# Optimization experiments

Measured on AMD Instinct MI355X. Metric: run time of the kernel, lower is better.

Reference implementation:

```python
import jax, jax.numpy as jnp
import numpy as np

B, N2, N3, D = 16, 1024, 2048, 128


def setup_inputs() -> dict:
    key = jax.random.key(0)
    k1, k2 = jax.random.split(key)
    desc2d = jax.random.normal(k1, (B * N2, D), dtype=jnp.float32)
    desc3d = jax.random.normal(k2, (B * N3, D), dtype=jnp.float32)
    # uniform, sorted batch ids (equal-size segments -> jit-friendly ragged layout)
    idx2d = jnp.repeat(jnp.arange(B, dtype=jnp.int64), N2)
    idx3d = jnp.repeat(jnp.arange(B, dtype=jnp.int64), N3)
    return {"desc2d": desc2d, "idx2d": idx2d, "desc3d": desc3d, "idx3d": idx3d}


def reference(desc2d, idx2d, desc3d, idx3d):
    # number of batches from sorted batch ids (static, computed on host)
    nb = int(np.asarray(idx2d)[-1]) + 1
    n2 = desc2d.shape[0] // nb
    n3 = desc3d.shape[0] // nb
    d2 = desc2d.reshape(nb, n2, -1)  # [B, n2, D]
    d3 = desc3d.reshape(nb, n3, -1)  # [B, n3, D]
    d2 = d2 / jnp.linalg.norm(d2, axis=-1, keepdims=True)
    d3 = d3 / jnp.linalg.norm(d3, axis=-1, keepdims=True)
    sim = jnp.einsum('bid,bjd->bij', d3, d2)  # cosine similarity [B, n3, n2]
    # zero-pad one extra row and column per batch (dustbin), as in the original
    return jnp.pad(sim, ((0, 0), (0, 1), (0, 1)))
```

## Files before the change

kernel.cpp:

```cpp
#include <hip/hip_runtime.h>
#include <hip/hip_bf16.h>

#define NB   16
#define N2   1024
#define N3   2048
#define DD   128
#define OROWS (N3 + 1)
#define OCOLS (N2 + 1)

typedef __attribute__((ext_vector_type(8))) __bf16 bf16x8;
typedef __attribute__((ext_vector_type(4))) float  f32x4;

static __device__ __forceinline__ unsigned pack_bf16x2(float a, float b) {
    unsigned ua = __float_as_uint(a);
    ua = (ua + 0x7FFF + ((ua >> 16) & 1)) >> 16;
    unsigned ub = __float_as_uint(b);
    ub = (ub + 0x7FFF + ((ub >> 16) & 1)) & 0xFFFF0000u;
    return ua | ub;
}

__global__ __launch_bounds__(512, 1)
void fused_kernel(const float* __restrict__ d2,
                  const float* __restrict__ d3,
                  float* __restrict__ out) {
    __shared__ __align__(16) char smem[65536];

    const int hw  = blockIdx.x;
    const int blk = (hw & 7) * 32 + (hw >> 3);
    const int b   = blk >> 4;
    const int ti  = blk & 15;

    const int t = threadIdx.x;

    const float* gA = d3 + ((size_t)(b * N3 + ti * 128)) * DD;
    const float* gB = d2 + ((size_t)b * N2) * DD;

    const int arow  = t >> 2;
    const int apart = t & 3;
    float4 av[8];
    #pragma unroll
    for (int i = 0; i < 8; ++i)
        av[i] = *reinterpret_cast<const float4*>(gA + (size_t)arow * DD + apart * 32 + i * 4);

    const int brow  = t >> 3;
    const int bpart = t & 7;
    float4 bv[4];
    #pragma unroll
    for (int i = 0; i < 4; ++i)
        bv[i] = *reinterpret_cast<const float4*>(gB + (size_t)brow * DD + bpart * 16 + i * 4);

    {
        float ss = 0.f;
        #pragma unroll
        for (int i = 0; i < 8; ++i)
            ss += av[i].x * av[i].x + av[i].y * av[i].y + av[i].z * av[i].z + av[i].w * av[i].w;
        ss += __shfl_xor(ss, 1);
        ss += __shfl_xor(ss, 2);
        const float s = rsqrtf(ss);
        const int aswz = (arow & 7) << 4;
        #pragma unroll
        for (int j = 0; j < 4; ++j) {
            uint4 w;
            w.x = pack_bf16x2(av[2*j].x * s,   av[2*j].y * s);
            w.y = pack_bf16x2(av[2*j].z * s,   av[2*j].w * s);
            w.z = pack_bf16x2(av[2*j+1].x * s, av[2*j+1].y * s);
            w.w = pack_bf16x2(av[2*j+1].z * s, av[2*j+1].w * s);
            int colb = apart * 64 + j * 16;
            *reinterpret_cast<uint4*>(smem + arow * 256 + (colb ^ aswz)) = w;
        }
    }
    {
        float ss = 0.f;
        #pragma unroll
        for (int i = 0; i < 4; ++i)
            ss += bv[i].x * bv[i].x + bv[i].y * bv[i].y + bv[i].z * bv[i].z + bv[i].w * bv[i].w;
        ss += __shfl_xor(ss, 1);
        ss += __shfl_xor(ss, 2);
        ss += __shfl_xor(ss, 4);
        const float s = rsqrtf(ss);
        const int bswz = (brow & 7) << 4;
        #pragma unroll
        for (int j = 0; j < 2; ++j) {
            uint4 w;
            w.x = pack_bf16x2(bv[2*j].x * s,   bv[2*j].y * s);
            w.y = pack_bf16x2(bv[2*j].z * s,   bv[2*j].w * s);
            w.z = pack_bf16x2(bv[2*j+1].x * s, bv[2*j+1].y * s);
            w.w = pack_bf16x2(bv[2*j+1].z * s, bv[2*j+1].w * s);
            int colb = bpart * 32 + j * 16;
            *reinterpret_cast<uint4*>(smem + 32768 + brow * 256 + (colb ^ bswz)) = w;
        }
    }
    asm volatile("s_waitcnt lgkmcnt(0)" ::: "memory");
    __builtin_amdgcn_s_barrier();
    __builtin_amdgcn_sched_barrier(0);

    const int wid = t >> 6;
    const int l   = t & 63;
    const int wm  = (wid >> 2) * 64;
    const int wn  = (wid & 3) * 16;
    const int lr  = l & 15;
    const int kq  = l >> 4;
    const int sw  = (lr & 7) << 4;

    bf16x8 af[4][4];
    #pragma unroll
    for (int ks = 0; ks < 4; ++ks) {
        const int kb = ks * 64 + kq * 16;
        #pragma unroll
        for (int mi = 0; mi < 4; ++mi) {
            int r = wm + mi * 16 + lr;
            af[ks][mi] = *reinterpret_cast<const bf16x8*>(smem + r * 256 + (kb ^ sw));
        }
    }

    float* obase = out + (size_t)b * OROWS * OCOLS + (size_t)(ti * 128) * OCOLS;

    for (int nj = 0; nj < 16; ++nj) {
        if (nj < 15) {
            const float* gc = gB + (size_t)(nj + 1) * 64 * DD;
            #pragma unroll
            for (int i = 0; i < 4; ++i)
                bv[i] = *reinterpret_cast<const float4*>(gc + (size_t)brow * DD + bpart * 16 + i * 4);
        }

        const char* bbuf = smem + 32768 + (nj & 1) * 16384;
        f32x4 acc[4] = {};
        #pragma unroll
        for (int ks = 0; ks < 4; ++ks) {
            const int kb = ks * 64 + kq * 16;
            bf16x8 bfr = *reinterpret_cast<const bf16x8*>(bbuf + (wn + lr) * 256 + (kb ^ sw));
            #pragma unroll
            for (int mi = 0; mi < 4; ++mi)
                acc[mi] = __builtin_amdgcn_mfma_f32_16x16x32_bf16(
                    af[ks][mi], bfr, acc[mi], 0, 0, 0);
        }

        #pragma unroll
        for (int mi = 0; mi < 4; ++mi) {
            #pragma unroll
            for (int i = 0; i < 4; ++i) {
                int r = wm + mi * 16 + kq * 4 + i;
                int c = nj * 64 + wn + lr;
                obase[(size_t)r * OCOLS + c] = acc[mi][i];
            }
        }

        if (nj < 15) {
            float ss = 0.f;
            #pragma unroll
            for (int i = 0; i < 4; ++i)
                ss += bv[i].x * bv[i].x + bv[i].y * bv[i].y + bv[i].z * bv[i].z + bv[i].w * bv[i].w;
            ss += __shfl_xor(ss, 1);
            ss += __shfl_xor(ss, 2);
            ss += __shfl_xor(ss, 4);
            const float s = rsqrtf(ss);
            const int bswz = (brow & 7) << 4;
            char* nb = smem + 32768 + ((nj + 1) & 1) * 16384;
            #pragma unroll
            for (int j = 0; j < 2; ++j) {
                uint4 w;
                w.x = pack_bf16x2(bv[2*j].x * s,   bv[2*j].y * s);
                w.y = pack_bf16x2(bv[2*j].z * s,   bv[2*j].w * s);
                w.z = pack_bf16x2(bv[2*j+1].x * s, bv[2*j+1].y * s);
                w.w = pack_bf16x2(bv[2*j+1].z * s, bv[2*j+1].w * s);
                int colb = bpart * 32 + j * 16;
                *reinterpret_cast<uint4*>(nb + brow * 256 + (colb ^ bswz)) = w;
            }
            asm volatile("s_waitcnt lgkmcnt(0)" ::: "memory");
        }
        asm volatile("" ::: "memory");
        __builtin_amdgcn_s_barrier();
        __builtin_amdgcn_sched_barrier(0);
    }

    if (t < 128)
        obase[(size_t)t * OCOLS + N2] = 0.0f;
    if (ti == 15) {
        float* last = out + (size_t)b * OROWS * OCOLS + (size_t)N3 * OCOLS;
        for (int c = t; c < OCOLS; c += 512) last[c] = 0.0f;
    }
}

extern "C" void kernel_launch(void* const* d_in, const int* in_sizes, int n_in,
                              void* d_out, int out_size, void* d_ws, size_t ws_size,
                              hipStream_t stream) {
    (void)in_sizes; (void)n_in; (void)out_size; (void)d_ws; (void)ws_size;
    const float* desc2d = (const float*)d_in[0];
    const float* desc3d = (const float*)d_in[2];
    float* out = (float*)d_out;

    fused_kernel<<<NB * (N3 / 128), 512, 0, stream>>>(desc2d, desc3d, out);
}
```

Before: 44.03 us.

## Load B fragments directly into registers, removing LDS staging and per-tile barriers

Each lane now loads its own B-operand slice straight from global memory in MFMA fragment layout. It normalizes the slice with a cross-lane shuffle reduction and packs it to bf16 in registers, so the B tile no longer goes through LDS. This removes the per-iteration LDS writes, the lgkmcnt waits and the workgroup barriers, and halves the LDS footprint. In exchange, each of the two waves sharing a wn column slice loads and normalizes the same B rows, doubling B global traffic (mostly L2 hits). The loop is unrolled by two with register double buffering, which raises register pressure.

```diff
diff --git a/kernel.cpp b/kernel.cpp
--- a/kernel.cpp
+++ b/kernel.cpp
@@ -23,17 +23,25 @@
 void fused_kernel(const float* __restrict__ d2,
                   const float* __restrict__ d3,
                   float* __restrict__ out) {
-    __shared__ __align__(16) char smem[65536];
+    __shared__ __align__(16) char smem[32768];
 
     const int hw  = blockIdx.x;
     const int blk = (hw & 7) * 32 + (hw >> 3);
     const int b   = blk >> 4;
     const int ti  = blk & 15;
+    const int t   = threadIdx.x;
 
-    const int t = threadIdx.x;
+    const int wid = t >> 6;
+    const int l   = t & 63;
+    const int wm  = (wid >> 2) * 64;
+    const int wn  = (wid & 3) * 16;
+    const int lr  = l & 15;
+    const int kq  = l >> 4;
+    const int sw  = (lr & 7) << 4;
 
-    const float* gA = d3 + ((size_t)(b * N3 + ti * 128)) * DD;
-    const float* gB = d2 + ((size_t)b * N2) * DD;
+    const float* gA  = d3 + ((size_t)(b * N3 + ti * 128)) * DD;
+    const float* gB  = d2 + ((size_t)b * N2) * DD;
+    const float* gBl = gB + (size_t)(wn + lr) * DD + kq * 8;
 
     const int arow  = t >> 2;
     const int apart = t & 3;
@@ -42,12 +50,12 @@
     for (int i = 0; i < 8; ++i)
         av[i] = *reinterpret_cast<const float4*>(gA + (size_t)arow * DD + apart * 32 + i * 4);
 
-    const int brow  = t >> 3;
-    const int bpart = t & 7;
-    float4 bv[4];
+    float4 bva[8], bvb[8];
     #pragma unroll
-    for (int i = 0; i < 4; ++i)
-        bv[i] = *reinterpret_cast<const float4*>(gB + (size_t)brow * DD + bpart * 16 + i * 4);
+    for (int ks = 0; ks < 4; ++ks) {
+        bva[ks * 2]     = *reinterpret_cast<const float4*>(gBl + ks * 32);
+        bva[ks * 2 + 1] = *reinterpret_cast<const float4*>(gBl + ks * 32 + 4);
+    }
 
     {
         float ss = 0.f;
@@ -61,46 +69,15 @@
         #pragma unroll
         for (int j = 0; j < 4; ++j) {
             uint4 w;
-            w.x = pack_bf16x2(av[2*j].x * s,   av[2*j].y * s);
-            w.y = pack_bf16x2(av[2*j].z * s,   av[2*j].w * s);
-            w.z = pack_bf16x2(av[2*j+1].x * s, av[2*j+1].y * s);
-            w.w = pack_bf16x2(av[2*j+1].z * s, av[2*j+1].w * s);
+            w.x = pack_bf16x2(av[2 * j].x * s,     av[2 * j].y * s);
+            w.y = pack_bf16x2(av[2 * j].z * s,     av[2 * j].w * s);
+            w.z = pack_bf16x2(av[2 * j + 1].x * s, av[2 * j + 1].y * s);
+            w.w = pack_bf16x2(av[2 * j + 1].z * s, av[2 * j + 1].w * s);
             int colb = apart * 64 + j * 16;
             *reinterpret_cast<uint4*>(smem + arow * 256 + (colb ^ aswz)) = w;
         }
     }
-    {
-        float ss = 0.f;
-        #pragma unroll
-        for (int i = 0; i < 4; ++i)
-            ss += bv[i].x * bv[i].x + bv[i].y * bv[i].y + bv[i].z * bv[i].z + bv[i].w * bv[i].w;
-        ss += __shfl_xor(ss, 1);
-        ss += __shfl_xor(ss, 2);
-        ss += __shfl_xor(ss, 4);
-        const float s = rsqrtf(ss);
-        const int bswz = (brow & 7) << 4;
-        #pragma unroll
-        for (int j = 0; j < 2; ++j) {
-            uint4 w;
-            w.x = pack_bf16x2(bv[2*j].x * s,   bv[2*j].y * s);
-            w.y = pack_bf16x2(bv[2*j].z * s,   bv[2*j].w * s);
-            w.z = pack_bf16x2(bv[2*j+1].x * s, bv[2*j+1].y * s);
-            w.w = pack_bf16x2(bv[2*j+1].z * s, bv[2*j+1].w * s);
-            int colb = bpart * 32 + j * 16;
-            *reinterpret_cast<uint4*>(smem + 32768 + brow * 256 + (colb ^ bswz)) = w;
-        }
-    }
-    asm volatile("s_waitcnt lgkmcnt(0)" ::: "memory");
-    __builtin_amdgcn_s_barrier();
-    __builtin_amdgcn_sched_barrier(0);
-
-    const int wid = t >> 6;
-    const int l   = t & 63;
-    const int wm  = (wid >> 2) * 64;
-    const int wn  = (wid & 3) * 16;
-    const int lr  = l & 15;
-    const int kq  = l >> 4;
-    const int sw  = (lr & 7) << 4;
+    __syncthreads();
 
     bf16x8 af[4][4];
     #pragma unroll
@@ -115,20 +92,33 @@
 
     float* obase = out + (size_t)b * OROWS * OCOLS + (size_t)(ti * 128) * OCOLS;
 
-    for (int nj = 0; nj < 16; ++nj) {
-        if (nj < 15) {
-            const float* gc = gB + (size_t)(nj + 1) * 64 * DD;
-            #pragma unroll
-            for (int i = 0; i < 4; ++i)
-                bv[i] = *reinterpret_cast<const float4*>(gc + (size_t)brow * DD + bpart * 16 + i * 4);
+    auto loadB = [&](float4 (&dst)[8], int nj) {
+        const float* p = gBl + (size_t)nj * 64 * DD;
+        #pragma unroll
+        for (int ks = 0; ks < 4; ++ks) {
+            dst[ks * 2]     = *reinterpret_cast<const float4*>(p + ks * 32);
+            dst[ks * 2 + 1] = *reinterpret_cast<const float4*>(p + ks * 32 + 4);
         }
+    };
 
-        const char* bbuf = smem + 32768 + (nj & 1) * 16384;
+    auto process = [&](const float4 (&bv)[8], int nj) {
+        float ss = 0.f;
+        #pragma unroll
+        for (int i = 0; i < 8; ++i)
+            ss += bv[i].x * bv[i].x + bv[i].y * bv[i].y + bv[i].z * bv[i].z + bv[i].w * bv[i].w;
+        ss += __shfl_xor(ss, 16);
+        ss += __shfl_xor(ss, 32);
+        const float s = rsqrtf(ss);
+
         f32x4 acc[4] = {};
         #pragma unroll
         for (int ks = 0; ks < 4; ++ks) {
-            const int kb = ks * 64 + kq * 16;
-            bf16x8 bfr = *reinterpret_cast<const bf16x8*>(bbuf + (wn + lr) * 256 + (kb ^ sw));
+            uint4 w;
+            w.x = pack_bf16x2(bv[2 * ks].x * s,     bv[2 * ks].y * s);
+            w.y = pack_bf16x2(bv[2 * ks].z * s,     bv[2 * ks].w * s);
+            w.z = pack_bf16x2(bv[2 * ks + 1].x * s, bv[2 * ks + 1].y * s);
+            w.w = pack_bf16x2(bv[2 * ks + 1].z * s, bv[2 * ks + 1].w * s);
+            bf16x8 bfr = __builtin_bit_cast(bf16x8, w);
             #pragma unroll
             for (int mi = 0; mi < 4; ++mi)
                 acc[mi] = __builtin_amdgcn_mfma_f32_16x16x32_bf16(
@@ -144,33 +134,13 @@
                 obase[(size_t)r * OCOLS + c] = acc[mi][i];
             }
         }
+    };
 
-        if (nj < 15) {
-            float ss = 0.f;
-            #pragma unroll
-            for (int i = 0; i < 4; ++i)
-                ss += bv[i].x * bv[i].x + bv[i].y * bv[i].y + bv[i].z * bv[i].z + bv[i].w * bv[i].w;
-            ss += __shfl_xor(ss, 1);
-            ss += __shfl_xor(ss, 2);
-            ss += __shfl_xor(ss, 4);
-            const float s = rsqrtf(ss);
-            const int bswz = (brow & 7) << 4;
-            char* nb = smem + 32768 + ((nj + 1) & 1) * 16384;
-            #pragma unroll
-            for (int j = 0; j < 2; ++j) {
-                uint4 w;
-                w.x = pack_bf16x2(bv[2*j].x * s,   bv[2*j].y * s);
-                w.y = pack_bf16x2(bv[2*j].z * s,   bv[2*j].w * s);
-                w.z = pack_bf16x2(bv[2*j+1].x * s, bv[2*j+1].y * s);
-                w.w = pack_bf16x2(bv[2*j+1].z * s, bv[2*j+1].w * s);
-                int colb = bpart * 32 + j * 16;
-                *reinterpret_cast<uint4*>(nb + brow * 256 + (colb ^ bswz)) = w;
-            }
-            asm volatile("s_waitcnt lgkmcnt(0)" ::: "memory");
-        }
-        asm volatile("" ::: "memory");
-        __builtin_amdgcn_s_barrier();
-        __builtin_amdgcn_sched_barrier(0);
+    for (int nj = 0; nj < 16; nj += 2) {
+        loadB(bvb, nj + 1);
+        process(bva, nj);
+        if (nj + 2 < 16) loadB(bva, nj + 2);
+        process(bvb, nj + 1);
     }
 
     if (t < 128)
```

After: 53.27 us. 1.21x slower.
